# Optimization experiments

Hardware: AMD Instinct MI355X
Metric: run time of the kernel (lower is better)

## Reference

```python
import jax, jax.numpy as jnp
import numpy as np

B, T, D, H = 2, 2048, 768, 12
HD = D // H  # head_dim = 64


def setup_inputs() -> dict:
    key = jax.random.key(0)
    ks = jax.random.split(key, 5)
    s = 0.02
    return {
        "x": jax.random.normal(ks[0], (B, T, D), dtype=jnp.float32),
        "w_qkv": jax.random.normal(ks[1], (D, 3 * D), dtype=jnp.float32) * s,
        "b_qkv": jax.random.normal(ks[2], (3 * D,), dtype=jnp.float32) * s,
        "w_out": jax.random.normal(ks[3], (D, D), dtype=jnp.float32) * s,
        "b_out": jax.random.normal(ks[4], (D,), dtype=jnp.float32) * s,
    }


def reference(x, w_qkv, b_qkv, w_out, b_out):
    Bx, Tx, C = x.shape
    qkv = x @ w_qkv + b_qkv                       # [B,T,3C]
    q, k, v = jnp.split(qkv, 3, axis=-1)
    # [B,H,T,hd]
    q = q.reshape(Bx, Tx, H, HD).transpose(0, 2, 1, 3)
    k = k.reshape(Bx, Tx, H, HD).transpose(0, 2, 1, 3)
    v = v.reshape(Bx, Tx, H, HD).transpose(0, 2, 1, 3)
    scale = 1.0 / jnp.sqrt(jnp.float32(HD))
    attn = jnp.einsum('bhqd,bhkd->bhqk', q, k) * scale  # [B,H,T,T]
    causal = jnp.tril(jnp.ones((Tx, Tx), dtype=bool))
    attn = jnp.where(causal, attn, -jnp.inf)
    attn = jax.nn.softmax(attn, axis=-1)
    y = jnp.einsum('bhqk,bhkd->bhqd', attn, v)          # [B,H,T,hd]
    y = y.transpose(0, 2, 1, 3).reshape(Bx, Tx, C)
    return y @ w_out + b_out
```

## Files before the change

### kernel.cpp

```cpp
#include <hip/hip_runtime.h>
#include <math.h>

typedef __attribute__((ext_vector_type(8))) __bf16 bf16x8;
typedef __attribute__((ext_vector_type(4))) __bf16 bf16x4;
typedef __attribute__((ext_vector_type(4))) float f32x4;

#define GLOAD_LDS16(gsrc, ldst) \
  __builtin_amdgcn_global_load_lds((__attribute__((address_space(1))) const void*)(gsrc), \
                                   (__attribute__((address_space(3))) void*)(ldst), 16, 0, 0)

__device__ __forceinline__ float fexp2(float x) {
#if __has_builtin(__builtin_amdgcn_exp2f)
  return __builtin_amdgcn_exp2f(x);
#else
  return exp2f(x);
#endif
}

__global__ __launch_bounds__(256)
void cvt_fused_kernel(const float* __restrict__ x, __bf16* __restrict__ xb,
                      const float* __restrict__ wqkv, __bf16* __restrict__ wqkvT,
                      const float* __restrict__ wout, __bf16* __restrict__ woT) {
  __shared__ float t[32][33];
  const int bid = blockIdx.x;
  if (bid < 3072) {
    int i = bid * 256 + threadIdx.x;
    float4 f = ((const float4*)x)[i];
    bf16x4 o;
    o[0] = (__bf16)f.x; o[1] = (__bf16)f.y; o[2] = (__bf16)f.z; o[3] = (__bf16)f.w;
    ((bf16x4*)xb)[i] = o;
    return;
  }
  const float* in;
  __bf16* out;
  int R, C, bx, by;
  if (bid < 4800) {
    int tt = bid - 3072;
    bx = tt % 72; by = tt / 72;
    in = wqkv; out = wqkvT; R = 768; C = 2304;
  } else {
    int tt = bid - 4800;
    bx = tt % 24; by = tt / 24;
    in = wout; out = woT; R = 768; C = 768;
  }
  int c0 = bx * 32, r0 = by * 32;
  int tc = threadIdx.x & 31, tr = threadIdx.x >> 5;
#pragma unroll
  for (int i = 0; i < 4; ++i)
    t[tr + 8 * i][tc] = in[(size_t)(r0 + tr + 8 * i) * C + c0 + tc];
  __syncthreads();
#pragma unroll
  for (int i = 0; i < 4; ++i)
    out[(size_t)(c0 + tr + 8 * i) * R + r0 + tc] = (__bf16)t[tc][tr + 8 * i];
}

template<int EPI, int BM, int BN, int WAVES, int WGM, int WGN, int BUFS>
__global__ __launch_bounds__(WAVES * 64, 3)
void gemm_tn_kernel(const __bf16* __restrict__ A, const __bf16* __restrict__ Bm,
                    const float* __restrict__ bias, float* __restrict__ outF,
                    __bf16* __restrict__ qo, __bf16* __restrict__ ko, __bf16* __restrict__ vo,
                    int M, int N, int K, int NBX, int NNX, int PPX) {
  constexpr int NTA = BM / 16, NTB = BN / 16;
  constexpr int NA = 2 * NTA;
  constexpr int NSEG = 2 * NTA + 2 * NTB;
  constexpr int LPTH = (NSEG + WAVES - 1) / WAVES;
  constexpr int LPTR = NSEG % WAVES;
  constexpr int LLO = (LPTR == 0) ? LPTH : LPTH - 1;
  constexpr int AM = NTA / WGM;
  constexpr int BNF = NTB / WGN;
  const int lane = threadIdx.x & 63;
  const int wave = threadIdx.x >> 6;
  const int r16 = lane & 15, g = lane >> 4;
  const int id = blockIdx.x;
  const int xcd = id & 7, slot = id >> 3;
  const int nxn = NBX / NNX;
  const int mg = xcd / nxn, ng = xcd % nxn;
  const int lp = slot / NNX, ln = slot - (slot / NNX) * NNX;
  const int mBase = (mg * PPX + lp) * BM, nBase = (ng * NNX + ln) * BN;
  __shared__ __align__(16) __bf16 lds[BUFS][NSEG * 512];

  f32x4 acc[AM][BNF];
#pragma unroll
  for (int i = 0; i < AM; ++i)
#pragma unroll
    for (int j = 0; j < BNF; ++j) acc[i][j] = (f32x4){0.f, 0.f, 0.f, 0.f};

  const int mw = (wave / WGN) * AM;
  const int nw = (wave % WGN) * BNF;

  auto stage = [&](int ke, int b) {
#pragma unroll
    for (int i = 0; i < LPTH; ++i) {
      int s = wave + i * WAVES;
      if (LPTR == 0 || s < NSEG) {
        int isB = (s >= NA);
        int sb = isB ? s - NA : s;
        int nt = isB ? NTB : NTA;
        int ks = sb / nt, t8 = sb - ks * nt;
        int row = (isB ? nBase : mBase) + t8 * 16 + r16;
        const __bf16* src = (isB ? Bm : A) + (size_t)row * K + ke + ks * 32 + g * 8;
        GLOAD_LDS16(src, &lds[b][s * 512]);
      }
    }
  };

  auto mfma_step = [&](const __bf16* L) {
#pragma unroll
    for (int ks = 0; ks < 2; ++ks) {
      bf16x8 af[AM], bfr[BNF];
#pragma unroll
      for (int i = 0; i < AM; ++i)
        af[i] = *(const bf16x8*)&L[((ks * NTA + mw + i) * 64 + lane) * 8];
#pragma unroll
      for (int j = 0; j < BNF; ++j)
        bfr[j] = *(const bf16x8*)&L[((NA + ks * NTB + nw + j) * 64 + lane) * 8];
      __builtin_amdgcn_s_setprio(1);
#pragma unroll
      for (int i = 0; i < AM; ++i)
#pragma unroll
        for (int j = 0; j < BNF; ++j)
          acc[i][j] = __builtin_amdgcn_mfma_f32_16x16x32_bf16(af[i], bfr[j], acc[i][j], 0, 0, 0);
      __builtin_amdgcn_s_setprio(0);
    }
  };

  const int nt = K >> 6;
  if constexpr (BUFS == 2) {
    stage(0, 0);
    int cur = 0;
    for (int t = 0; t < nt; ++t) {
      __syncthreads();
      if (t + 1 < nt) stage((t + 1) << 6, cur ^ 1);
      mfma_step(lds[cur]);
      cur ^= 1;
    }
  } else {
    stage(0, 0);
    stage(64, 1);
    int cur = 0;
    for (int t = 0; t < nt; ++t) {
      if (t + 1 < nt) {
        if (LPTR != 0 && wave < LPTR) asm volatile("s_waitcnt vmcnt(%0)" :: "i"(LPTH) : "memory");
        else                          asm volatile("s_waitcnt vmcnt(%0)" :: "i"(LLO) : "memory");
      } else {
        asm volatile("s_waitcnt vmcnt(0)" ::: "memory");
      }
      __builtin_amdgcn_sched_barrier(0);
      __builtin_amdgcn_s_barrier();
      __builtin_amdgcn_sched_barrier(0);
      int nxt = cur + 2; if (nxt >= 3) nxt -= 3;
      if (t + 2 < nt) stage((t + 2) << 6, nxt);
      mfma_step(lds[cur]);
      if (++cur == 3) cur = 0;
    }
  }

#pragma unroll
  for (int i = 0; i < AM; ++i) {
#pragma unroll
    for (int j = 0; j < BNF; ++j) {
      int c = nBase + (nw + j) * 16 + r16;
      float bb = bias[c];
#pragma unroll
      for (int e = 0; e < 4; ++e) {
        int r = mBase + (mw + i) * 16 + g * 4 + e;
        float val = acc[i][j][e] + bb;
        if (EPI == 0) {
          int which = c / 768;
          int cc = c - which * 768;
          int hh = cc >> 6, dd = cc & 63;
          int bI = r >> 11, tt = r & 2047;
          if (which == 0) {
            qo[(((size_t)(bI * 12 + hh)) * 2048 + tt) * 64 + dd] = (__bf16)(val * 0.180336880f);
          } else if (which == 1) {
            ko[(((size_t)(bI * 12 + hh)) * 2048 + tt) * 64 + dd] = (__bf16)val;
          } else {
            vo[(((size_t)(bI * 12 + hh)) * 64 + dd) * 2048 + tt] = (__bf16)val;
          }
        } else {
          outF[(size_t)r * N + c] = val;
        }
      }
    }
  }
}

__global__ __launch_bounds__(256, 2)
void attn_kernel(const __bf16* __restrict__ qg, const __bf16* __restrict__ kg,
                 const __bf16* __restrict__ vtg, __bf16* __restrict__ yatt) {
  const int id = blockIdx.x;
  const int chunk = id & 7, within = id >> 3;
  const int bh = chunk * 3 + (within >> 5);
  const int a = within & 31, p = 63 - a;
  const int Ka = (a >> 1) + 1, Kp = (p >> 1) + 1;
  const int lane = threadIdx.x & 63, wave = threadIdx.x >> 6;
  const int r16 = lane & 15, g = lane >> 4;
  const int bI = bh / 12, h = bh - bI * 12;
  const size_t headoff = (size_t)bh * 2048 * 64;
  const __bf16* Q = qg + headoff;
  const __bf16* Kh = kg + headoff;
  const __bf16* VT = vtg + headoff;

  __shared__ __align__(16) __bf16 Kbuf[2][4096];
  __shared__ __align__(16) __bf16 Vbuf[2][4096];
  __shared__ __align__(16) __bf16 Plds[4][16][72];

  const int myTile = (wave < 2) ? p : a;
  const int myKt   = (wave < 2) ? Kp : Ka;
  const int rowQ   = myTile * 32 + (wave & 1) * 16 + r16;

  bf16x8 qf[2];
#pragma unroll
  for (int ks = 0; ks < 2; ++ks)
    qf[ks] = *(const bf16x8*)&Q[(size_t)rowQ * 64 + ks * 32 + g * 8];

  int srow[2], scl[2];
#pragma unroll
  for (int i = 0; i < 2; ++i) {
    int c = (i * 4 + wave) * 64 + lane;
    srow[i] = c >> 3;
    scl[i] = (c & 7) ^ (srow[i] & 7);
  }
  auto stage = [&](int kt, int b) {
#pragma unroll
    for (int i = 0; i < 2; ++i) {
      GLOAD_LDS16(&Kh[(size_t)(kt * 64 + srow[i]) * 64 + scl[i] * 8], &Kbuf[b][(i * 4 + wave) * 512]);
      GLOAD_LDS16(&VT[(size_t)srow[i] * 2048 + kt * 64 + scl[i] * 8], &Vbuf[b][(i * 4 + wave) * 512]);
    }
  };

  f32x4 o[4];
#pragma unroll
  for (int j = 0; j < 4; ++j) o[j] = (f32x4){0.f, 0.f, 0.f, 0.f};
  float l = 0.f;

  stage(0, 0);
  for (int kt = 0; kt < Kp; ++kt) {
    const int cur = kt & 1;
    __syncthreads();
    if (kt + 1 < Kp) stage(kt + 1, cur ^ 1);
    if (kt < myKt) {
      f32x4 st[4];
#pragma unroll
      for (int j = 0; j < 4; ++j) st[j] = (f32x4){0.f, 0.f, 0.f, 0.f};
      __builtin_amdgcn_s_setprio(1);
#pragma unroll
      for (int ks = 0; ks < 2; ++ks)
#pragma unroll
        for (int j = 0; j < 4; ++j) {
          int row = j * 16 + r16;
          int cp = (ks * 4 + g) ^ (row & 7);
          bf16x8 kf = *(const bf16x8*)&Kbuf[cur][(row * 8 + cp) * 8];
          st[j] = __builtin_amdgcn_mfma_f32_16x16x32_bf16(kf, qf[ks], st[j], 0, 0, 0);
        }
      __builtin_amdgcn_s_setprio(0);
      bf16x8 vf[2][4];
#pragma unroll
      for (int ks = 0; ks < 2; ++ks)
#pragma unroll
        for (int dj = 0; dj < 4; ++dj) {
          int row = dj * 16 + r16;
          int cp = (ks * 4 + g) ^ (row & 7);
          vf[ks][dj] = *(const bf16x8*)&Vbuf[cur][(row * 8 + cp) * 8];
        }
      if (kt == myKt - 1) {
#pragma unroll
        for (int j = 0; j < 4; ++j)
#pragma unroll
          for (int e = 0; e < 4; ++e)
            if (kt * 64 + j * 16 + 4 * g + e > rowQ) st[j][e] = -INFINITY;
      }
      float ls = 0.f;
#pragma unroll
      for (int j = 0; j < 4; ++j)
#pragma unroll
        for (int e = 0; e < 4; ++e) {
          float pv = fexp2(st[j][e]);
          st[j][e] = pv;
          ls += pv;
        }
      ls += __shfl_xor(ls, 16, 64);
      ls += __shfl_xor(ls, 32, 64);
      l += ls;
#pragma unroll
      for (int j = 0; j < 4; ++j) {
        bf16x4 pk;
#pragma unroll
        for (int e = 0; e < 4; ++e) pk[e] = (__bf16)st[j][e];
        *(bf16x4*)&Plds[wave][r16][j * 16 + 4 * g] = pk;
      }
      __builtin_amdgcn_s_setprio(1);
#pragma unroll
      for (int ks = 0; ks < 2; ++ks) {
        bf16x8 pf = *(const bf16x8*)&Plds[wave][r16][ks * 32 + g * 8];
#pragma unroll
        for (int dj = 0; dj < 4; ++dj)
          o[dj] = __builtin_amdgcn_mfma_f32_16x16x32_bf16(vf[ks][dj], pf, o[dj], 0, 0, 0);
      }
      __builtin_amdgcn_s_setprio(0);
    }
  }

  float inv = 1.0f / l;
#pragma unroll
  for (int dj = 0; dj < 4; ++dj) {
    bf16x4 ov;
#pragma unroll
    for (int e = 0; e < 4; ++e) ov[e] = (__bf16)(o[dj][e] * inv);
    *(bf16x4*)&yatt[((size_t)(bI * 2048 + rowQ)) * 768 + h * 64 + dj * 16 + 4 * g] = ov;
  }
}

extern "C" void kernel_launch(void* const* d_in, const int* in_sizes, int n_in,
                              void* d_out, int out_size, void* d_ws, size_t ws_size,
                              hipStream_t stream) {
  (void)in_sizes; (void)n_in; (void)out_size; (void)ws_size;
  const float* x     = (const float*)d_in[0];
  const float* w_qkv = (const float*)d_in[1];
  const float* b_qkv = (const float*)d_in[2];
  const float* w_out = (const float*)d_in[3];
  const float* b_out = (const float*)d_in[4];
  float* out = (float*)d_out;

  char* ws = (char*)d_ws;
  __bf16* xb    = (__bf16*)(ws);
  __bf16* wqkvT = (__bf16*)(ws + 6291456);
  __bf16* woT   = (__bf16*)(ws + 9830400);
  __bf16* qb    = (__bf16*)(ws + 11010048);
  __bf16* kb    = (__bf16*)(ws + 17301504);
  __bf16* vtb   = (__bf16*)(ws + 23592960);
  __bf16* yatt  = (__bf16*)(ws + 29884416);

  cvt_fused_kernel<<<5376, 256, 0, stream>>>(x, xb, w_qkv, wqkvT, w_out, woT);
  gemm_tn_kernel<0, 128, 288, 12, 2, 6, 3><<<256, 768, 0, stream>>>(
      xb, wqkvT, b_qkv, nullptr, qb, kb, vtb, 4096, 2304, 768, 8, 1, 32);
  attn_kernel<<<768, 256, 0, stream>>>(qb, kb, vtb, yatt);
  gemm_tn_kernel<1, 64, 96, 4, 2, 2, 3><<<512, 256, 0, stream>>>(
      yatt, woT, b_out, out, nullptr, nullptr, nullptr, 4096, 768, 768, 8, 4, 16);
}
```

Before: 101.2 us.

## Add dedicated QKV GEMM with register-loaded A and LDS-staged B tiles

```diff
diff --git a/kernel.cpp b/kernel.cpp
--- a/kernel.cpp
+++ b/kernel.cpp
@@ -54,12 +54,115 @@
     out[(size_t)(c0 + tr + 8 * i) * R + r0 + tc] = (__bf16)t[tc][tr + 8 * i];
 }
 
-template<int EPI, int BM, int BN, int WAVES, int WGM, int WGN, int BUFS>
+__global__ __launch_bounds__(384, 3)
+void qkv_gemm_kernel(const __bf16* __restrict__ A, const __bf16* __restrict__ Bm,
+                     const float* __restrict__ bias,
+                     __bf16* __restrict__ qo, __bf16* __restrict__ ko, __bf16* __restrict__ vo) {
+  const int K = 768;
+  const int lane = threadIdx.x & 63, wave = threadIdx.x >> 6;
+  const int r16 = lane & 15, g = lane >> 4;
+  const int id = blockIdx.x;
+  const int xcd = id & 7, slot = id >> 3;
+  const int lp = slot >> 1, ln = slot & 1;
+  const int mBase = lp * 128, nBase = (xcd * 2 + ln) * 144;
+  __shared__ __align__(16) __bf16 lds[3][9216];
+
+  f32x4 acc[4][3];
+#pragma unroll
+  for (int i = 0; i < 4; ++i)
+#pragma unroll
+    for (int j = 0; j < 3; ++j) acc[i][j] = (f32x4){0.f, 0.f, 0.f, 0.f};
+
+  const int mw = (wave / 3) * 4;
+  const int nw = (wave % 3) * 3;
+
+  auto stageB = [&](int ke, int b) {
+#pragma unroll
+    for (int i = 0; i < 3; ++i) {
+      int s = wave + i * 6;
+      int ks = s / 9, t8 = s - ks * 9;
+      int row = nBase + t8 * 16 + r16;
+      GLOAD_LDS16(&Bm[(size_t)row * K + ke + ks * 32 + g * 8], &lds[b][s * 512]);
+    }
+  };
+  auto loadA = [&](int ke, bf16x8 (&af)[4][2]) {
+#pragma unroll
+    for (int i = 0; i < 4; ++i)
+#pragma unroll
+      for (int ks = 0; ks < 2; ++ks)
+        af[i][ks] = *(const bf16x8*)&A[(size_t)(mBase + (mw + i) * 16 + r16) * K + ke + ks * 32 + g * 8];
+  };
+  auto compute = [&](const __bf16* L, const bf16x8 (&af)[4][2]) {
+#pragma unroll
+    for (int ks = 0; ks < 2; ++ks) {
+      bf16x8 bfr[3];
+#pragma unroll
+      for (int j = 0; j < 3; ++j)
+        bfr[j] = *(const bf16x8*)&L[((ks * 9 + nw + j) * 64 + lane) * 8];
+      __builtin_amdgcn_s_setprio(1);
+#pragma unroll
+      for (int i = 0; i < 4; ++i)
+#pragma unroll
+        for (int j = 0; j < 3; ++j)
+          acc[i][j] = __builtin_amdgcn_mfma_f32_16x16x32_bf16(af[i][ks], bfr[j], acc[i][j], 0, 0, 0);
+      __builtin_amdgcn_s_setprio(0);
+    }
+  };
+
+  bf16x8 afE[4][2], afO[4][2];
+  stageB(0, 0);
+  loadA(0, afE);
+  stageB(64, 1);
+#pragma unroll 1
+  for (int t = 0; t < 12; t += 2) {
+    asm volatile("s_waitcnt vmcnt(3)" ::: "memory");
+    __builtin_amdgcn_sched_barrier(0);
+    __builtin_amdgcn_s_barrier();
+    __builtin_amdgcn_sched_barrier(0);
+    loadA((t + 1) << 6, afO);
+    if (t + 2 < 12) stageB((t + 2) << 6, (t + 2) % 3);
+    compute(lds[t % 3], afE);
+    if (t + 2 < 12) asm volatile("s_waitcnt vmcnt(3)" ::: "memory");
+    else            asm volatile("s_waitcnt vmcnt(0)" ::: "memory");
+    __builtin_amdgcn_sched_barrier(0);
+    __builtin_amdgcn_s_barrier();
+    __builtin_amdgcn_sched_barrier(0);
+    if (t + 2 < 12) loadA((t + 2) << 6, afE);
+    if (t + 3 < 12) stageB((t + 3) << 6, (t + 3) % 3);
+    compute(lds[(t + 1) % 3], afO);
+  }
+
+#pragma unroll
+  for (int i = 0; i < 4; ++i) {
+#pragma unroll
+    for (int j = 0; j < 3; ++j) {
+      int c = nBase + (nw + j) * 16 + r16;
+      float bb = bias[c];
+#pragma unroll
+      for (int e = 0; e < 4; ++e) {
+        int r = mBase + (mw + i) * 16 + g * 4 + e;
+        float val = acc[i][j][e] + bb;
+        int which = c / 768;
+        int cc = c - which * 768;
+        int hh = cc >> 6, dd = cc & 63;
+        int bI = r >> 11, tt = r & 2047;
+        if (which == 0) {
+          qo[(((size_t)(bI * 12 + hh)) * 2048 + tt) * 64 + dd] = (__bf16)(val * 0.180336880f);
+        } else if (which == 1) {
+          ko[(((size_t)(bI * 12 + hh)) * 2048 + tt) * 64 + dd] = (__bf16)val;
+        } else {
+          vo[(((size_t)(bI * 12 + hh)) * 64 + dd) * 2048 + tt] = (__bf16)val;
+        }
+      }
+    }
+  }
+}
+
+template<int BM, int BN, int WAVES, int WGM, int WGN>
 __global__ __launch_bounds__(WAVES * 64, 3)
-void gemm_tn_kernel(const __bf16* __restrict__ A, const __bf16* __restrict__ Bm,
-                    const float* __restrict__ bias, float* __restrict__ outF,
-                    __bf16* __restrict__ qo, __bf16* __restrict__ ko, __bf16* __restrict__ vo,
-                    int M, int N, int K, int NBX, int NNX, int PPX) {
+void gemm_out_kernel(const __bf16* __restrict__ A, const __bf16* __restrict__ Bm,
+                     const float* __restrict__ bias, float* __restrict__ outF,
+                     int M, int N, int K, int NBX, int NNX, int PPX) {
   constexpr int NTA = BM / 16, NTB = BN / 16;
   constexpr int NA = 2 * NTA;
   constexpr int NSEG = 2 * NTA + 2 * NTB;
@@ -77,7 +180,7 @@
   const int mg = xcd / nxn, ng = xcd % nxn;
   const int lp = slot / NNX, ln = slot - (slot / NNX) * NNX;
   const int mBase = (mg * PPX + lp) * BM, nBase = (ng * NNX + ln) * BN;
-  __shared__ __align__(16) __bf16 lds[BUFS][NSEG * 512];
+  __shared__ __align__(16) __bf16 lds[3][NSEG * 512];
 
   f32x4 acc[AM][BNF];
 #pragma unroll
@@ -125,34 +228,23 @@
   };
 
   const int nt = K >> 6;
-  if constexpr (BUFS == 2) {
-    stage(0, 0);
-    int cur = 0;
-    for (int t = 0; t < nt; ++t) {
-      __syncthreads();
-      if (t + 1 < nt) stage((t + 1) << 6, cur ^ 1);
-      mfma_step(lds[cur]);
-      cur ^= 1;
-    }
-  } else {
-    stage(0, 0);
-    stage(64, 1);
-    int cur = 0;
-    for (int t = 0; t < nt; ++t) {
-      if (t + 1 < nt) {
-        if (LPTR != 0 && wave < LPTR) asm volatile("s_waitcnt vmcnt(%0)" :: "i"(LPTH) : "memory");
-        else                          asm volatile("s_waitcnt vmcnt(%0)" :: "i"(LLO) : "memory");
-      } else {
-        asm volatile("s_waitcnt vmcnt(0)" ::: "memory");
-      }
-      __builtin_amdgcn_sched_barrier(0);
-      __builtin_amdgcn_s_barrier();
-      __builtin_amdgcn_sched_barrier(0);
-      int nxt = cur + 2; if (nxt >= 3) nxt -= 3;
-      if (t + 2 < nt) stage((t + 2) << 6, nxt);
-      mfma_step(lds[cur]);
-      if (++cur == 3) cur = 0;
-    }
+  stage(0, 0);
+  stage(64, 1);
+  int cur = 0;
+  for (int t = 0; t < nt; ++t) {
+    if (t + 1 < nt) {
+      if (LPTR != 0 && wave < LPTR) asm volatile("s_waitcnt vmcnt(%0)" :: "i"(LPTH) : "memory");
+      else                          asm volatile("s_waitcnt vmcnt(%0)" :: "i"(LLO) : "memory");
+    } else {
+      asm volatile("s_waitcnt vmcnt(0)" ::: "memory");
+    }
+    __builtin_amdgcn_sched_barrier(0);
+    __builtin_amdgcn_s_barrier();
+    __builtin_amdgcn_sched_barrier(0);
+    int nxt = cur + 2; if (nxt >= 3) nxt -= 3;
+    if (t + 2 < nt) stage((t + 2) << 6, nxt);
+    mfma_step(lds[cur]);
+    if (++cur == 3) cur = 0;
   }
 
 #pragma unroll
@@ -164,22 +256,7 @@
 #pragma unroll
       for (int e = 0; e < 4; ++e) {
         int r = mBase + (mw + i) * 16 + g * 4 + e;
-        float val = acc[i][j][e] + bb;
-        if (EPI == 0) {
-          int which = c / 768;
-          int cc = c - which * 768;
-          int hh = cc >> 6, dd = cc & 63;
-          int bI = r >> 11, tt = r & 2047;
-          if (which == 0) {
-            qo[(((size_t)(bI * 12 + hh)) * 2048 + tt) * 64 + dd] = (__bf16)(val * 0.180336880f);
-          } else if (which == 1) {
-            ko[(((size_t)(bI * 12 + hh)) * 2048 + tt) * 64 + dd] = (__bf16)val;
-          } else {
-            vo[(((size_t)(bI * 12 + hh)) * 64 + dd) * 2048 + tt] = (__bf16)val;
-          }
-        } else {
-          outF[(size_t)r * N + c] = val;
-        }
+        outF[(size_t)r * N + c] = acc[i][j][e] + bb;
       }
     }
   }
@@ -332,9 +409,8 @@
   __bf16* yatt  = (__bf16*)(ws + 29884416);
 
   cvt_fused_kernel<<<5376, 256, 0, stream>>>(x, xb, w_qkv, wqkvT, w_out, woT);
-  gemm_tn_kernel<0, 128, 288, 12, 2, 6, 3><<<256, 768, 0, stream>>>(
-      xb, wqkvT, b_qkv, nullptr, qb, kb, vtb, 4096, 2304, 768, 8, 1, 32);
+  qkv_gemm_kernel<<<512, 384, 0, stream>>>(xb, wqkvT, b_qkv, qb, kb, vtb);
   attn_kernel<<<768, 256, 0, stream>>>(qb, kb, vtb, yatt);
-  gemm_tn_kernel<1, 64, 96, 4, 2, 2, 3><<<512, 256, 0, stream>>>(
-      yatt, woT, b_out, out, nullptr, nullptr, nullptr, 4096, 768, 768, 8, 4, 16);
-}
+  gemm_out_kernel<64, 96, 4, 2, 2><<<512, 256, 0, stream>>>(
+      yatt, woT, b_out, out, 4096, 768, 768, 8, 4, 16);
+}
```

Result: slower. 148.9 us (+47.1%).
